# Kernel tuning notes

Hardware: AMD Instinct MI355X
Metric: run time of the kernel (lower is better)

Reference implementation:

```python
import jax, jax.numpy as jnp
import numpy as np

N_NODES = 50000
N_EDGES = 800000


def sage_conv(x, src, dst, W_l, b_l, W_r, num_nodes):
    """PyG SAGEConv with mean aggregation: out = lin_l(mean_agg(neighbors)) + lin_r(x)."""
    # gather source-node features per edge, scatter-mean into destination nodes
    msg = x[src]                                                   # [E, F]
    agg = jax.ops.segment_sum(msg, dst, num_segments=num_nodes)    # [N, F]
    cnt = jax.ops.segment_sum(jnp.ones((src.shape[0],), x.dtype), dst,
                              num_segments=num_nodes)              # [N]
    agg = agg / jnp.maximum(cnt, 1.0)[:, None]
    return agg @ W_l + b_l + x @ W_r


def setup_inputs() -> dict:
    key = jax.random.key(0)
    ks = jax.random.split(key, 8)
    d_in, d_hid, d_out = 128, 256, 128
    s = lambda k, shape, fan: jax.random.normal(k, shape, jnp.float32) / np.sqrt(fan)
    return {
        "x": jax.random.normal(ks[0], (N_NODES, d_in), jnp.float32),
        "edge_index": jax.random.randint(ks[1], (2, N_EDGES), 0, N_NODES, jnp.int64),
        "W1_l": s(ks[2], (d_in, d_hid), d_in),
        "b1": jnp.zeros((d_hid,), jnp.float32),
        "W1_r": s(ks[3], (d_in, d_hid), d_in),
        "W2_l": s(ks[4], (d_hid, d_out), d_hid),
        "b2": jnp.zeros((d_out,), jnp.float32),
        "W2_r": s(ks[5], (d_hid, d_out), d_hid),
    }


def reference(x, edge_index, W1_l, b1, W1_r, W2_l, b2, W2_r):
    src, dst = edge_index[0], edge_index[1]
    n = x.shape[0]
    h = sage_conv(x, src, dst, W1_l, b1, W1_r, n)
    h = jax.nn.relu(h)  # dropout p=0.0 -> identity
    out = sage_conv(h, src, dst, W2_l, b2, W2_r, n)
    return out
```

## Files before the change

kernel.cpp:

```cpp
#include <hip/hip_runtime.h>
#include <hip/hip_bf16.h>
#include <stdint.h>

#define NN 50000
#define NE 800000
#define NB 196
#define EPB 2048
#define NBLK ((NE + EPB - 1) / EPB)

typedef __attribute__((ext_vector_type(8))) __bf16 bf16x8;
typedef __attribute__((ext_vector_type(4))) float f32x4;
typedef __attribute__((ext_vector_type(4))) int i32x4;

__device__ __forceinline__ float bflo(uint32_t u) { return __uint_as_float(u << 16); }
__device__ __forceinline__ float bfhi(uint32_t u) { return __uint_as_float(u & 0xffff0000u); }
__device__ __forceinline__ uint16_t f2bf(float f) {
    uint32_t u = __float_as_uint(f);
    u += 0x7fffu + ((u >> 16) & 1u);
    return (uint16_t)(u >> 16);
}
__device__ __forceinline__ float bf2f(uint16_t h) { return __uint_as_float(((uint32_t)h) << 16); }

__device__ __forceinline__ int xcd_swz(int bid, int nwg) {
    int q = nwg >> 3, r = nwg & 7;
    int xcd = bid & 7, idx = bid >> 3;
    int base = (xcd < r) ? xcd * (q + 1) : r * (q + 1) + (xcd - r) * q;
    return base + idx;
}

__device__ __forceinline__ int detect_i64(const int* ei, int* sh_cnt) {
    int t = threadIdx.x;
    if (t == 0) *sh_cnt = 0;
    __syncthreads();
    if (t < 64) atomicAdd(sh_cnt, (ei[2 * t + 1] != 0) ? 1 : 0);
    __syncthreads();
    return (*sh_cnt < 4) ? 1 : 0;
}

__device__ __forceinline__ int detect_fp32(const uint32_t* xu, int* sh_cnt) {
    int t = threadIdx.x;
    if (t == 0) *sh_cnt = 0;
    __syncthreads();
    uint32_t u = xu[t & 255];
    uint32_t lo = u & 0xffffu;
    uint32_t e = (lo >> 7) & 0xffu;
    int ok = (lo == 0u) || (e >= 96u && e <= 150u);
    if (t < 256) atomicAdd(sh_cnt, ok);
    __syncthreads();
    return (*sh_cnt < 192) ? 1 : 0;
}

__global__ __launch_bounds__(256) void hist_pass(const int* __restrict__ ei,
                                                 int* __restrict__ histM) {
    __shared__ int hist[NB];
    __shared__ int shc;
    int fl = detect_i64(ei, &shc);
    for (int i = threadIdx.x; i < NB; i += 256) hist[i] = 0;
    __syncthreads();
    int base = blockIdx.x * EPB;
    for (int i = 0; i < EPB; i += 256) {
        int e = base + i + threadIdx.x;
        if (e < NE) {
            int d = fl ? ei[2 * NE + 2 * e] : ei[NE + e];
            atomicAdd(&hist[d >> 8], 1);
        }
    }
    __syncthreads();
    for (int i = threadIdx.x; i < NB; i += 256) histM[i * NBLK + blockIdx.x] = hist[i];
}

__global__ __launch_bounds__(512) void scan_rows(int* __restrict__ histM, int* __restrict__ bucket_tot) {
    __shared__ int sm[512];
    int b = blockIdx.x, t = threadIdx.x;
    int v = (t < NBLK) ? histM[b * NBLK + t] : 0;
    sm[t] = v;
    __syncthreads();
    for (int o = 1; o < 512; o <<= 1) {
        int x = (t >= o) ? sm[t - o] : 0;
        __syncthreads();
        sm[t] += x;
        __syncthreads();
    }
    if (t < NBLK) histM[b * NBLK + t] = sm[t] - v;
    if (t == 511) bucket_tot[b] = sm[511];
}

__global__ __launch_bounds__(256) void scatter_pass(const int* __restrict__ ei,
                                                    const int* __restrict__ histM,
                                                    const int* __restrict__ bucket_tot,
                                                    uint32_t* __restrict__ staging) {
    __shared__ int sm[256];
    __shared__ int curs[NB];
    __shared__ int shc;
    int fl = detect_i64(ei, &shc);
    int blk = blockIdx.x, t = threadIdx.x;
    int v = (t < NB) ? bucket_tot[t] : 0;
    sm[t] = v;
    __syncthreads();
    for (int o = 1; o < 256; o <<= 1) {
        int x = (t >= o) ? sm[t - o] : 0;
        __syncthreads();
        sm[t] += x;
        __syncthreads();
    }
    if (t < NB) curs[t] = (sm[t] - v) + histM[t * NBLK + blk];
    __syncthreads();
    int base = blk * EPB;
    for (int i = 0; i < EPB; i += 256) {
        int e = base + i + t;
        if (e < NE) {
            int s, d;
            if (fl) { s = ei[2 * e]; d = ei[2 * NE + 2 * e]; }
            else    { s = ei[e];     d = ei[NE + e]; }
            int p = atomicAdd(&curs[d >> 8], 1);
            staging[p] = ((uint32_t)(d & 0xff) << 16) | (uint32_t)s;
        }
    }
}

__global__ __launch_bounds__(256) void build_csr(const uint32_t* __restrict__ staging,
                                                 const int* __restrict__ bucket_tot,
                                                 int* __restrict__ row_start, int* __restrict__ deg,
                                                 float* __restrict__ inv_deg, int* __restrict__ csr) {
    __shared__ int degs[256];
    __shared__ int sm[256];
    __shared__ int curs[256];
    __shared__ int beg_s, cnt_s;
    int b = blockIdx.x, t = threadIdx.x;
    int v = (t < NB) ? bucket_tot[t] : 0;
    sm[t] = v;
    __syncthreads();
    for (int o = 1; o < 256; o <<= 1) {
        int x = (t >= o) ? sm[t - o] : 0;
        __syncthreads();
        sm[t] += x;
        __syncthreads();
    }
    if (t == b) { beg_s = sm[t] - v; cnt_s = v; }
    __syncthreads();
    int beg = beg_s, cnt = cnt_s;
    degs[t] = 0;
    __syncthreads();
    for (int i = t; i < cnt; i += 256) atomicAdd(&degs[(staging[beg + i] >> 16) & 0xff], 1);
    __syncthreads();
    int d = degs[t];
    sm[t] = d;
    __syncthreads();
    for (int o = 1; o < 256; o <<= 1) {
        int x = (t >= o) ? sm[t - o] : 0;
        __syncthreads();
        sm[t] += x;
        __syncthreads();
    }
    int excl = sm[t] - d;
    curs[t] = excl;
    int node = b * 256 + t;
    if (node < NN) {
        row_start[node] = beg + excl;
        deg[node] = d;
        inv_deg[node] = 1.0f / (float)(d > 0 ? d : 1);
    }
    __syncthreads();
    for (int i = t; i < cnt; i += 256) {
        uint32_t u = staging[beg + i];
        int dl = (u >> 16) & 0xff;
        int p = atomicAdd(&curs[dl], 1);
        csr[beg + p] = (int)(u & 0xffffu);
    }
}

#define NORMX_BLKS 6250
__global__ __launch_bounds__(256) void norm_all(const void* __restrict__ x,
                                                const void* __restrict__ w1l, const void* __restrict__ b1,
                                                const void* __restrict__ w1r, const void* __restrict__ w2l,
                                                const void* __restrict__ b2, const void* __restrict__ w2r,
                                                uint32_t* __restrict__ xb,
                                                uint16_t* __restrict__ w1l_sw, uint16_t* __restrict__ w1r_sw,
                                                uint16_t* __restrict__ w2l_sw, uint16_t* __restrict__ w2r_sw,
                                                uint16_t* __restrict__ bias_buf) {
    __shared__ int shc;
    int fp32 = detect_fp32((const uint32_t*)x, &shc);
    if (blockIdx.x < NORMX_BLKS) {
        int i = blockIdx.x * 256 + threadIdx.x;
        if (fp32) {
            f32x4 v = ((const f32x4*)x)[i];
            uint2 o;
            o.x = (uint32_t)f2bf(v[0]) | ((uint32_t)f2bf(v[1]) << 16);
            o.y = (uint32_t)f2bf(v[2]) | ((uint32_t)f2bf(v[3]) << 16);
            ((uint2*)xb)[i] = o;
        } else {
            ((uint2*)xb)[i] = ((const uint2*)x)[i];
        }
        return;
    }
    int tid = (blockIdx.x - NORMX_BLKS) * 256 + threadIdx.x;
    if (tid < 16384) {
        int frag = tid >> 6, lane = tid & 63;
        const void* srcw; uint16_t* dst; int N; int fl;
        if (frag < 64)       { srcw = w1l; dst = w1l_sw; N = 256; fl = frag; }
        else if (frag < 128) { srcw = w1r; dst = w1r_sw; N = 256; fl = frag - 64; }
        else if (frag < 192) { srcw = w2l; dst = w2l_sw; N = 128; fl = frag - 128; }
        else                 { srcw = w2r; dst = w2r_sw; N = 128; fl = frag - 192; }
        int NTm = N >> 4;
        int kt = fl / NTm, nt = fl - kt * NTm;
        int k0 = kt * 32 + (lane >> 4) * 8, n = nt * 16 + (lane & 15);
        uint16_t* d = dst + (size_t)fl * 512 + lane * 8;
#pragma unroll
        for (int j = 0; j < 8; j++) {
            int si = (k0 + j) * N + n;
            d[j] = fp32 ? f2bf(((const float*)srcw)[si]) : ((const uint16_t*)srcw)[si];
        }
    } else if (tid < 16384 + 384) {
        int j = tid - 16384;
        const void* s = (j < 256) ? b1 : b2;
        int jj = (j < 256) ? j : j - 256;
        bias_buf[j] = fp32 ? f2bf(((const float*)s)[jj]) : ((const uint16_t*)s)[jj];
    }
}

__global__ __launch_bounds__(256) void agg_mean_v2(const uint32_t* __restrict__ xu,
                                                   const int* __restrict__ row_start,
                                                   const int* __restrict__ deg,
                                                   const int* __restrict__ csr,
                                                   const float* __restrict__ inv_deg,
                                                   uint32_t* __restrict__ outu) {
    int wave = threadIdx.x >> 6, lane = threadIdx.x & 63;
    int half = lane >> 5, l = lane & 31;
    int node = blockIdx.x * 8 + wave * 2 + half;
    int beg = row_start[node], end = beg + deg[node];
    float lx[8], hx[8], ly[8], hy[8];
#pragma unroll
    for (int k = 0; k < 8; k++) { lx[k] = 0.f; hx[k] = 0.f; ly[k] = 0.f; hy[k] = 0.f; }
    int j = beg;
    for (; j + 8 <= end; j += 8) {
        int idx[8];
#pragma unroll
        for (int k = 0; k < 8; k++) idx[k] = csr[j + k];
#pragma unroll
        for (int k = 0; k < 8; k++) {
            uint2 v = *(const uint2*)(xu + (size_t)idx[k] * 64 + l * 2);
            lx[k] += bflo(v.x); hx[k] += bfhi(v.x);
            ly[k] += bflo(v.y); hy[k] += bfhi(v.y);
        }
    }
    for (; j < end; j++) {
        uint2 v = *(const uint2*)(xu + (size_t)csr[j] * 64 + l * 2);
        lx[0] += bflo(v.x); hx[0] += bfhi(v.x);
        ly[0] += bflo(v.y); hy[0] += bfhi(v.y);
    }
    float sc = inv_deg[node];
    float r0 = (((lx[0] + lx[1]) + (lx[2] + lx[3])) + ((lx[4] + lx[5]) + (lx[6] + lx[7]))) * sc;
    float r1 = (((hx[0] + hx[1]) + (hx[2] + hx[3])) + ((hx[4] + hx[5]) + (hx[6] + hx[7]))) * sc;
    float r2 = (((ly[0] + ly[1]) + (ly[2] + ly[3])) + ((ly[4] + ly[5]) + (ly[6] + ly[7]))) * sc;
    float r3 = (((hy[0] + hy[1]) + (hy[2] + hy[3])) + ((hy[4] + hy[5]) + (hy[6] + hy[7]))) * sc;
    uint2 o;
    o.x = (uint32_t)f2bf(r0) | ((uint32_t)f2bf(r1) << 16);
    o.y = (uint32_t)f2bf(r2) | ((uint32_t)f2bf(r3) << 16);
    *(uint2*)(outu + (size_t)node * 64 + l * 2) = o;
}

__global__ __launch_bounds__(256) void agg_final_v2(const uint32_t* __restrict__ tu,
                                                    const int* __restrict__ row_start,
                                                    const int* __restrict__ deg,
                                                    const int* __restrict__ csr,
                                                    const float* __restrict__ inv_deg,
                                                    const f32x4* __restrict__ u,
                                                    f32x4* __restrict__ out) {
    int wave = threadIdx.x >> 6, lane = threadIdx.x & 63;
    int half = lane >> 5, l = lane & 31;
    int node = blockIdx.x * 8 + wave * 2 + half;
    int beg = row_start[node], end = beg + deg[node];
    float lx[8], hx[8], ly[8], hy[8];
#pragma unroll
    for (int k = 0; k < 8; k++) { lx[k] = 0.f; hx[k] = 0.f; ly[k] = 0.f; hy[k] = 0.f; }
    int j = beg;
    for (; j + 8 <= end; j += 8) {
        int idx[8];
#pragma unroll
        for (int k = 0; k < 8; k++) idx[k] = csr[j + k];
#pragma unroll
        for (int k = 0; k < 8; k++) {
            uint2 v = *(const uint2*)(tu + (size_t)idx[k] * 64 + l * 2);
            lx[k] += bflo(v.x); hx[k] += bfhi(v.x);
            ly[k] += bflo(v.y); hy[k] += bfhi(v.y);
        }
    }
    for (; j < end; j++) {
        uint2 v = *(const uint2*)(tu + (size_t)csr[j] * 64 + l * 2);
        lx[0] += bflo(v.x); hx[0] += bfhi(v.x);
        ly[0] += bflo(v.y); hy[0] += bfhi(v.y);
    }
    float sc = inv_deg[node];
    f32x4 uv = u[(size_t)node * 32 + l];
    f32x4 r;
    r[0] = (((lx[0] + lx[1]) + (lx[2] + lx[3])) + ((lx[4] + lx[5]) + (lx[6] + lx[7]))) * sc + uv[0];
    r[1] = (((hx[0] + hx[1]) + (hx[2] + hx[3])) + ((hx[4] + hx[5]) + (hx[6] + hx[7]))) * sc + uv[1];
    r[2] = (((ly[0] + ly[1]) + (ly[2] + ly[3])) + ((ly[4] + ly[5]) + (ly[6] + ly[7]))) * sc + uv[2];
    r[3] = (((hy[0] + hy[1]) + (hy[2] + hy[3])) + ((hy[4] + hy[5]) + (hy[6] + hy[7]))) * sc + uv[3];
    out[(size_t)node * 32 + l] = r;
}

__global__ __launch_bounds__(256) void gemm1_v3(const uint16_t* __restrict__ A1,
                                                const uint16_t* __restrict__ A2,
                                                const uint16_t* __restrict__ W1sw,
                                                const uint16_t* __restrict__ W2sw,
                                                const uint16_t* __restrict__ bias,
                                                uint16_t* __restrict__ C) {
    __shared__ __align__(16) uint16_t cs[64][72];
    int wg = xcd_swz(blockIdx.x, 3128);
    int rg = wg >> 2, cg = wg & 3;
    int wave = threadIdx.x >> 6, lane = threadIdx.x & 63;
    int wr = wave >> 1, wc = wave & 1;
    int m = lane & 15, q = lane >> 4;
    int rowbase = rg * 64 + wr * 32;
    int gnt0 = cg * 4 + wc * 2;

    int ar[2];
#pragma unroll
    for (int rf = 0; rf < 2; rf++) {
        int r = rowbase + rf * 16 + m;
        ar[rf] = (r < NN) ? r : (NN - 1);
    }

    bf16x8 B1[4][2], B2[4][2];
#pragma unroll
    for (int kt = 0; kt < 4; kt++)
#pragma unroll
        for (int nt = 0; nt < 2; nt++) {
            B1[kt][nt] = *(const bf16x8*)(W1sw + ((size_t)(kt * 16 + gnt0 + nt)) * 512 + lane * 8);
            B2[kt][nt] = *(const bf16x8*)(W2sw + ((size_t)(kt * 16 + gnt0 + nt)) * 512 + lane * 8);
        }

    f32x4 acc[2][2];
#pragma unroll
    for (int rf = 0; rf < 2; rf++)
#pragma unroll
        for (int nt = 0; nt < 2; nt++)
#pragma unroll
            for (int i = 0; i < 4; i++) acc[rf][nt][i] = 0.f;

#pragma unroll
    for (int kt = 0; kt < 4; kt++) {
        bf16x8 a10 = *(const bf16x8*)(A1 + (size_t)ar[0] * 128 + kt * 32 + q * 8);
        bf16x8 a11 = *(const bf16x8*)(A1 + (size_t)ar[1] * 128 + kt * 32 + q * 8);
        bf16x8 a20 = *(const bf16x8*)(A2 + (size_t)ar[0] * 128 + kt * 32 + q * 8);
        bf16x8 a21 = *(const bf16x8*)(A2 + (size_t)ar[1] * 128 + kt * 32 + q * 8);
#pragma unroll
        for (int nt = 0; nt < 2; nt++) {
            acc[0][nt] = __builtin_amdgcn_mfma_f32_16x16x32_bf16(a10, B1[kt][nt], acc[0][nt], 0, 0, 0);
            acc[1][nt] = __builtin_amdgcn_mfma_f32_16x16x32_bf16(a11, B1[kt][nt], acc[1][nt], 0, 0, 0);
            acc[0][nt] = __builtin_amdgcn_mfma_f32_16x16x32_bf16(a20, B2[kt][nt], acc[0][nt], 0, 0, 0);
            acc[1][nt] = __builtin_amdgcn_mfma_f32_16x16x32_bf16(a21, B2[kt][nt], acc[1][nt], 0, 0, 0);
        }
    }

#pragma unroll
    for (int rf = 0; rf < 2; rf++)
#pragma unroll
        for (int nt = 0; nt < 2; nt++) {
            int coll = wc * 32 + nt * 16 + m;
            float bv = bf2f(bias[cg * 64 + coll]);
#pragma unroll
            for (int i = 0; i < 4; i++) {
                float v = fmaxf(acc[rf][nt][i] + bv, 0.f);
                cs[wr * 32 + rf * 16 + q * 4 + i][coll] = f2bf(v);
            }
        }
    __syncthreads();
    int tt = threadIdx.x;
#pragma unroll
    for (int rr = 0; rr < 2; rr++) {
        int row = rr * 32 + (tt >> 3);
        int grow = rg * 64 + row;
        if (grow < NN)
            *(i32x4*)(C + (size_t)grow * 256 + cg * 64 + (tt & 7) * 8) =
                *(const i32x4*)&cs[row][(tt & 7) * 8];
    }
}

__global__ __launch_bounds__(256) void gemm2_v3(const uint16_t* __restrict__ A,
                                                const uint16_t* __restrict__ W1sw,
                                                const uint16_t* __restrict__ W2sw,
                                                const uint16_t* __restrict__ bias,
                                                uint16_t* __restrict__ T,
                                                float* __restrict__ U) {
    __shared__ __align__(16) uint16_t ts[64][72];
    __shared__ __align__(16) float us[64][68];
    int wg = xcd_swz(blockIdx.x, 1564);
    int rg = wg >> 1, cg = wg & 1;
    int wave = threadIdx.x >> 6, lane = threadIdx.x & 63;
    int wr = wave >> 1, wc = wave & 1;
    int m = lane & 15, q = lane >> 4;
    int rowbase = rg * 64 + wr * 32;
    int gnt0 = cg * 4 + wc * 2;

    int ar[2];
#pragma unroll
    for (int rf = 0; rf < 2; rf++) {
        int r = rowbase + rf * 16 + m;
        ar[rf] = (r < NN) ? r : (NN - 1);
    }

    f32x4 acc1[2][2], acc2[2][2];
#pragma unroll
    for (int rf = 0; rf < 2; rf++)
#pragma unroll
        for (int nt = 0; nt < 2; nt++)
#pragma unroll
            for (int i = 0; i < 4; i++) { acc1[rf][nt][i] = 0.f; acc2[rf][nt][i] = 0.f; }

#pragma unroll
    for (int kt = 0; kt < 8; kt++) {
        bf16x8 b10 = *(const bf16x8*)(W1sw + ((size_t)(kt * 8 + gnt0 + 0)) * 512 + lane * 8);
        bf16x8 b11 = *(const bf16x8*)(W1sw + ((size_t)(kt * 8 + gnt0 + 1)) * 512 + lane * 8);
        bf16x8 b20 = *(const bf16x8*)(W2sw + ((size_t)(kt * 8 + gnt0 + 0)) * 512 + lane * 8);
        bf16x8 b21 = *(const bf16x8*)(W2sw + ((size_t)(kt * 8 + gnt0 + 1)) * 512 + lane * 8);
        bf16x8 a0 = *(const bf16x8*)(A + (size_t)ar[0] * 256 + kt * 32 + q * 8);
        bf16x8 a1 = *(const bf16x8*)(A + (size_t)ar[1] * 256 + kt * 32 + q * 8);
        acc1[0][0] = __builtin_amdgcn_mfma_f32_16x16x32_bf16(a0, b10, acc1[0][0], 0, 0, 0);
        acc1[0][1] = __builtin_amdgcn_mfma_f32_16x16x32_bf16(a0, b11, acc1[0][1], 0, 0, 0);
        acc1[1][0] = __builtin_amdgcn_mfma_f32_16x16x32_bf16(a1, b10, acc1[1][0], 0, 0, 0);
        acc1[1][1] = __builtin_amdgcn_mfma_f32_16x16x32_bf16(a1, b11, acc1[1][1], 0, 0, 0);
        acc2[0][0] = __builtin_amdgcn_mfma_f32_16x16x32_bf16(a0, b20, acc2[0][0], 0, 0, 0);
        acc2[0][1] = __builtin_amdgcn_mfma_f32_16x16x32_bf16(a0, b21, acc2[0][1], 0, 0, 0);
        acc2[1][0] = __builtin_amdgcn_mfma_f32_16x16x32_bf16(a1, b20, acc2[1][0], 0, 0, 0);
        acc2[1][1] = __builtin_amdgcn_mfma_f32_16x16x32_bf16(a1, b21, acc2[1][1], 0, 0, 0);
    }

#pragma unroll
    for (int rf = 0; rf < 2; rf++)
#pragma unroll
        for (int nt = 0; nt < 2; nt++) {
            int coll = wc * 32 + nt * 16 + m;
            float bv = bf2f(bias[cg * 64 + coll]);
#pragma unroll
            for (int i = 0; i < 4; i++) {
                int rl = wr * 32 + rf * 16 + q * 4 + i;
                ts[rl][coll] = f2bf(acc1[rf][nt][i]);
                us[rl][coll] = acc2[rf][nt][i] + bv;
            }
        }
    __syncthreads();
    int tt = threadIdx.x;
#pragma unroll
    for (int rr = 0; rr < 2; rr++) {
        int row = rr * 32 + (tt >> 3);
        int grow = rg * 64 + row;
        if (grow < NN)
            *(i32x4*)(T + (size_t)grow * 128 + cg * 64 + (tt & 7) * 8) =
                *(const i32x4*)&ts[row][(tt & 7) * 8];
    }
#pragma unroll
    for (int rr = 0; rr < 4; rr++) {
        int row = rr * 16 + (tt >> 4);
        int grow = rg * 64 + row;
        if (grow < NN)
            *(f32x4*)(U + (size_t)grow * 128 + cg * 64 + (tt & 15) * 4) =
                *(const f32x4*)&us[row][(tt & 15) * 4];
    }
}

extern "C" void kernel_launch(void* const* d_in, const int* in_sizes, int n_in,
                              void* d_out, int out_size, void* d_ws, size_t ws_size,
                              hipStream_t stream) {
    const void* x_raw  = d_in[0];
    const int*  ei     = (const int*)d_in[1];
    const void* W1l    = d_in[2];
    const void* b1     = d_in[3];
    const void* W1r    = d_in[4];
    const void* W2l    = d_in[5];
    const void* b2     = d_in[6];
    const void* W2r    = d_in[7];

    uint8_t* ws = (uint8_t*)d_ws;
    size_t off = 0;
    auto alloc = [&](size_t b) -> void* {
        void* p = ws + off;
        off += (b + 255) & ~(size_t)255;
        return p;
    };
    int*      histM       = (int*)alloc((size_t)NB * NBLK * 4);
    int*      bucket_tot  = (int*)alloc((NB + 4) * 4);
    int*      deg         = (int*)alloc((size_t)NN * 4);
    float*    inv_deg     = (float*)alloc((size_t)NN * 4);
    int*      row_start   = (int*)alloc((size_t)NN * 4);
    int*      csr         = (int*)alloc((size_t)NE * 4);
    uint32_t* xb          = (uint32_t*)alloc((size_t)NN * 64 * 4);
    uint16_t* bias_buf    = (uint16_t*)alloc(384 * 2);
    uint16_t* agg         = (uint16_t*)alloc((size_t)NN * 128 * 2);
    uint16_t* h           = (uint16_t*)alloc((size_t)NN * 256 * 2);
    uint16_t* t           = (uint16_t*)alloc((size_t)NN * 128 * 2);
    float*    u           = (float*)alloc((size_t)NN * 128 * 4);
    uint16_t* w1l_sw      = (uint16_t*)alloc(128 * 256 * 2);
    uint16_t* w1r_sw      = (uint16_t*)alloc(128 * 256 * 2);
    uint16_t* w2l_sw      = (uint16_t*)alloc(256 * 128 * 2);
    uint16_t* w2r_sw      = (uint16_t*)alloc(256 * 128 * 2);

    uint32_t* staging = (uint32_t*)h;

    hist_pass<<<NBLK, 256, 0, stream>>>(ei, histM);
    scan_rows<<<NB, 512, 0, stream>>>(histM, bucket_tot);
    scatter_pass<<<NBLK, 256, 0, stream>>>(ei, histM, bucket_tot, staging);
    build_csr<<<NB, 256, 0, stream>>>(staging, bucket_tot, row_start, deg, inv_deg, csr);

    norm_all<<<NORMX_BLKS + 66, 256, 0, stream>>>(x_raw, W1l, b1, W1r, W2l, b2, W2r,
                                                  xb, w1l_sw, w1r_sw, w2l_sw, w2r_sw, bias_buf);

    agg_mean_v2<<<NN / 8, 256, 0, stream>>>(xb, row_start, deg, csr, inv_deg, (uint32_t*)agg);
    gemm1_v3<<<3128, 256, 0, stream>>>(agg, (const uint16_t*)xb, w1l_sw, w1r_sw, bias_buf, h);
    gemm2_v3<<<1564, 256, 0, stream>>>(h, w2l_sw, w2r_sw, bias_buf + 256, t, u);
    agg_final_v2<<<NN / 8, 256, 0, stream>>>((const uint32_t*)t, row_start, deg, csr, inv_deg,
                                             (const f32x4*)u, (f32x4*)d_out);
}
```

Baseline: 268.3 us.

## Fuse layer-1 mean aggregation into the first GEMM via shared-memory tile

Replaces the separate agg_mean and gemm1 kernels with one kernel. Each 64-node block first gathers and averages neighbour features into a shared-memory tile, then runs the MFMA GEMM against both weight matrices, covering all 256 output columns per block. This removes the global round-trip of the aggregated matrix and one launch. In exchange the grid shrinks to about 782 blocks, weights are reloaded per k-step instead of held in registers, and the gather phase interleaves two nodes per half-wave, which raises register pressure and could lower occupancy.

```diff
diff --git a/kernel.cpp b/kernel.cpp
--- a/kernel.cpp
+++ b/kernel.cpp
@@ -218,163 +218,167 @@
     }
 }
 
-__global__ __launch_bounds__(256) void agg_mean_v2(const uint32_t* __restrict__ xu,
-                                                   const int* __restrict__ row_start,
-                                                   const int* __restrict__ deg,
-                                                   const int* __restrict__ csr,
-                                                   const float* __restrict__ inv_deg,
-                                                   uint32_t* __restrict__ outu) {
-    int wave = threadIdx.x >> 6, lane = threadIdx.x & 63;
-    int half = lane >> 5, l = lane & 31;
-    int node = blockIdx.x * 8 + wave * 2 + half;
-    int beg = row_start[node], end = beg + deg[node];
-    float lx[8], hx[8], ly[8], hy[8];
-#pragma unroll
-    for (int k = 0; k < 8; k++) { lx[k] = 0.f; hx[k] = 0.f; ly[k] = 0.f; hy[k] = 0.f; }
-    int j = beg;
-    for (; j + 8 <= end; j += 8) {
-        int idx[8];
-#pragma unroll
-        for (int k = 0; k < 8; k++) idx[k] = csr[j + k];
-#pragma unroll
-        for (int k = 0; k < 8; k++) {
-            uint2 v = *(const uint2*)(xu + (size_t)idx[k] * 64 + l * 2);
-            lx[k] += bflo(v.x); hx[k] += bfhi(v.x);
-            ly[k] += bflo(v.y); hy[k] += bfhi(v.y);
-        }
-    }
-    for (; j < end; j++) {
-        uint2 v = *(const uint2*)(xu + (size_t)csr[j] * 64 + l * 2);
-        lx[0] += bflo(v.x); hx[0] += bfhi(v.x);
-        ly[0] += bflo(v.y); hy[0] += bfhi(v.y);
-    }
-    float sc = inv_deg[node];
-    float r0 = (((lx[0] + lx[1]) + (lx[2] + lx[3])) + ((lx[4] + lx[5]) + (lx[6] + lx[7]))) * sc;
-    float r1 = (((hx[0] + hx[1]) + (hx[2] + hx[3])) + ((hx[4] + hx[5]) + (hx[6] + hx[7]))) * sc;
-    float r2 = (((ly[0] + ly[1]) + (ly[2] + ly[3])) + ((ly[4] + ly[5]) + (ly[6] + ly[7]))) * sc;
-    float r3 = (((hy[0] + hy[1]) + (hy[2] + hy[3])) + ((hy[4] + hy[5]) + (hy[6] + hy[7]))) * sc;
-    uint2 o;
-    o.x = (uint32_t)f2bf(r0) | ((uint32_t)f2bf(r1) << 16);
-    o.y = (uint32_t)f2bf(r2) | ((uint32_t)f2bf(r3) << 16);
-    *(uint2*)(outu + (size_t)node * 64 + l * 2) = o;
-}
-
-__global__ __launch_bounds__(256) void agg_final_v2(const uint32_t* __restrict__ tu,
-                                                    const int* __restrict__ row_start,
-                                                    const int* __restrict__ deg,
-                                                    const int* __restrict__ csr,
-                                                    const float* __restrict__ inv_deg,
-                                                    const f32x4* __restrict__ u,
-                                                    f32x4* __restrict__ out) {
-    int wave = threadIdx.x >> 6, lane = threadIdx.x & 63;
-    int half = lane >> 5, l = lane & 31;
-    int node = blockIdx.x * 8 + wave * 2 + half;
-    int beg = row_start[node], end = beg + deg[node];
-    float lx[8], hx[8], ly[8], hy[8];
-#pragma unroll
-    for (int k = 0; k < 8; k++) { lx[k] = 0.f; hx[k] = 0.f; ly[k] = 0.f; hy[k] = 0.f; }
-    int j = beg;
-    for (; j + 8 <= end; j += 8) {
-        int idx[8];
-#pragma unroll
-        for (int k = 0; k < 8; k++) idx[k] = csr[j + k];
-#pragma unroll
-        for (int k = 0; k < 8; k++) {
-            uint2 v = *(const uint2*)(tu + (size_t)idx[k] * 64 + l * 2);
-            lx[k] += bflo(v.x); hx[k] += bfhi(v.x);
-            ly[k] += bflo(v.y); hy[k] += bfhi(v.y);
-        }
-    }
-    for (; j < end; j++) {
-        uint2 v = *(const uint2*)(tu + (size_t)csr[j] * 64 + l * 2);
-        lx[0] += bflo(v.x); hx[0] += bfhi(v.x);
-        ly[0] += bflo(v.y); hy[0] += bfhi(v.y);
-    }
-    float sc = inv_deg[node];
-    f32x4 uv = u[(size_t)node * 32 + l];
-    f32x4 r;
-    r[0] = (((lx[0] + lx[1]) + (lx[2] + lx[3])) + ((lx[4] + lx[5]) + (lx[6] + lx[7]))) * sc + uv[0];
-    r[1] = (((hx[0] + hx[1]) + (hx[2] + hx[3])) + ((hx[4] + hx[5]) + (hx[6] + hx[7]))) * sc + uv[1];
-    r[2] = (((ly[0] + ly[1]) + (ly[2] + ly[3])) + ((ly[4] + ly[5]) + (ly[6] + ly[7]))) * sc + uv[2];
-    r[3] = (((hy[0] + hy[1]) + (hy[2] + hy[3])) + ((hy[4] + hy[5]) + (hy[6] + hy[7]))) * sc + uv[3];
-    out[(size_t)node * 32 + l] = r;
-}
-
-__global__ __launch_bounds__(256) void gemm1_v3(const uint16_t* __restrict__ A1,
-                                                const uint16_t* __restrict__ A2,
+#define ATW 136
+__global__ __launch_bounds__(256) void fused_l1(const uint32_t* __restrict__ xu,
+                                                const int* __restrict__ row_start,
+                                                const int* __restrict__ deg,
+                                                const int* __restrict__ csr,
+                                                const float* __restrict__ inv_deg,
+                                                const uint16_t* __restrict__ xb16,
                                                 const uint16_t* __restrict__ W1sw,
                                                 const uint16_t* __restrict__ W2sw,
                                                 const uint16_t* __restrict__ bias,
-                                                uint16_t* __restrict__ C) {
-    __shared__ __align__(16) uint16_t cs[64][72];
-    int wg = xcd_swz(blockIdx.x, 3128);
-    int rg = wg >> 2, cg = wg & 3;
-    int wave = threadIdx.x >> 6, lane = threadIdx.x & 63;
+                                                uint16_t* __restrict__ H) {
+    __shared__ __align__(16) uint16_t atile[64][ATW];
+    __shared__ __align__(16) uint16_t stg[64][136];
+    int node0 = blockIdx.x * 64;
+    int tid = threadIdx.x;
+    int wave = tid >> 6, lane = tid & 63;
+    int half = lane >> 5, l = lane & 31;
+
+    for (int pp = 0; pp < 4; pp++) {
+        int nlA = wave * 16 + pp * 4 + half * 2;
+        int nlB = nlA + 1;
+        int na = node0 + nlA; na = (na < NN) ? na : (NN - 1);
+        int nb = node0 + nlB; nb = (nb < NN) ? nb : (NN - 1);
+        int begA = row_start[na], endA = begA + deg[na];
+        int begB = row_start[nb], endB = begB + deg[nb];
+        float alx[8], ahx[8], aly[8], ahy[8];
+        float blx[8], bhx[8], bly[8], bhy[8];
+#pragma unroll
+        for (int k = 0; k < 8; k++) {
+            alx[k] = 0.f; ahx[k] = 0.f; aly[k] = 0.f; ahy[k] = 0.f;
+            blx[k] = 0.f; bhx[k] = 0.f; bly[k] = 0.f; bhy[k] = 0.f;
+        }
+        int ja = begA, jb = begB;
+        for (; ja + 8 <= endA && jb + 8 <= endB; ja += 8, jb += 8) {
+            int ia[8], ib[8];
+#pragma unroll
+            for (int k = 0; k < 8; k++) { ia[k] = csr[ja + k]; ib[k] = csr[jb + k]; }
+#pragma unroll
+            for (int k = 0; k < 8; k++) {
+                uint2 va = *(const uint2*)(xu + (size_t)ia[k] * 64 + l * 2);
+                uint2 vb = *(const uint2*)(xu + (size_t)ib[k] * 64 + l * 2);
+                alx[k] += bflo(va.x); ahx[k] += bfhi(va.x);
+                aly[k] += bflo(va.y); ahy[k] += bfhi(va.y);
+                blx[k] += bflo(vb.x); bhx[k] += bfhi(vb.x);
+                bly[k] += bflo(vb.y); bhy[k] += bfhi(vb.y);
+            }
+        }
+        for (; ja + 8 <= endA; ja += 8) {
+            int ia[8];
+#pragma unroll
+            for (int k = 0; k < 8; k++) ia[k] = csr[ja + k];
+#pragma unroll
+            for (int k = 0; k < 8; k++) {
+                uint2 va = *(const uint2*)(xu + (size_t)ia[k] * 64 + l * 2);
+                alx[k] += bflo(va.x); ahx[k] += bfhi(va.x);
+                aly[k] += bflo(va.y); ahy[k] += bfhi(va.y);
+            }
+        }
+        for (; jb + 8 <= endB; jb += 8) {
+            int ib[8];
+#pragma unroll
+            for (int k = 0; k < 8; k++) ib[k] = csr[jb + k];
+#pragma unroll
+            for (int k = 0; k < 8; k++) {
+                uint2 vb = *(const uint2*)(xu + (size_t)ib[k] * 64 + l * 2);
+                blx[k] += bflo(vb.x); bhx[k] += bfhi(vb.x);
+                bly[k] += bflo(vb.y); bhy[k] += bfhi(vb.y);
+            }
+        }
+        for (; ja < endA; ja++) {
+            uint2 va = *(const uint2*)(xu + (size_t)csr[ja] * 64 + l * 2);
+            alx[0] += bflo(va.x); ahx[0] += bfhi(va.x);
+            aly[0] += bflo(va.y); ahy[0] += bfhi(va.y);
+        }
+        for (; jb < endB; jb++) {
+            uint2 vb = *(const uint2*)(xu + (size_t)csr[jb] * 64 + l * 2);
+            blx[0] += bflo(vb.x); bhx[0] += bfhi(vb.x);
+            bly[0] += bflo(vb.y); bhy[0] += bfhi(vb.y);
+        }
+        float sa = inv_deg[na], sb = inv_deg[nb];
+        float a0 = (((alx[0] + alx[1]) + (alx[2] + alx[3])) + ((alx[4] + alx[5]) + (alx[6] + alx[7]))) * sa;
+        float a1 = (((ahx[0] + ahx[1]) + (ahx[2] + ahx[3])) + ((ahx[4] + ahx[5]) + (ahx[6] + ahx[7]))) * sa;
+        float a2 = (((aly[0] + aly[1]) + (aly[2] + aly[3])) + ((aly[4] + aly[5]) + (aly[6] + aly[7]))) * sa;
+        float a3 = (((ahy[0] + ahy[1]) + (ahy[2] + ahy[3])) + ((ahy[4] + ahy[5]) + (ahy[6] + ahy[7]))) * sa;
+        float b0 = (((blx[0] + blx[1]) + (blx[2] + blx[3])) + ((blx[4] + blx[5]) + (blx[6] + blx[7]))) * sb;
+        float b1v = (((bhx[0] + bhx[1]) + (bhx[2] + bhx[3])) + ((bhx[4] + bhx[5]) + (bhx[6] + bhx[7]))) * sb;
+        float b2v = (((bly[0] + bly[1]) + (bly[2] + bly[3])) + ((bly[4] + bly[5]) + (bly[6] + bly[7]))) * sb;
+        float b3 = (((bhy[0] + bhy[1]) + (bhy[2] + bhy[3])) + ((bhy[4] + bhy[5]) + (bhy[6] + bhy[7]))) * sb;
+        uint2 oa, ob;
+        oa.x = (uint32_t)f2bf(a0) | ((uint32_t)f2bf(a1) << 16);
+        oa.y = (uint32_t)f2bf(a2) | ((uint32_t)f2bf(a3) << 16);
+        ob.x = (uint32_t)f2bf(b0) | ((uint32_t)f2bf(b1v) << 16);
+        ob.y = (uint32_t)f2bf(b2v) | ((uint32_t)f2bf(b3) << 16);
+        *(uint2*)((char*)&atile[nlA][0] + l * 8) = oa;
+        *(uint2*)((char*)&atile[nlB][0] + l * 8) = ob;
+    }
+    __syncthreads();
+
     int wr = wave >> 1, wc = wave & 1;
     int m = lane & 15, q = lane >> 4;
-    int rowbase = rg * 64 + wr * 32;
-    int gnt0 = cg * 4 + wc * 2;
-
     int ar[2];
 #pragma unroll
     for (int rf = 0; rf < 2; rf++) {
-        int r = rowbase + rf * 16 + m;
+        int r = node0 + wr * 32 + rf * 16 + m;
         ar[rf] = (r < NN) ? r : (NN - 1);
     }
-
-    bf16x8 B1[4][2], B2[4][2];
-#pragma unroll
-    for (int kt = 0; kt < 4; kt++)
-#pragma unroll
-        for (int nt = 0; nt < 2; nt++) {
-            B1[kt][nt] = *(const bf16x8*)(W1sw + ((size_t)(kt * 16 + gnt0 + nt)) * 512 + lane * 8);
-            B2[kt][nt] = *(const bf16x8*)(W2sw + ((size_t)(kt * 16 + gnt0 + nt)) * 512 + lane * 8);
-        }
-
-    f32x4 acc[2][2];
+    f32x4 acc[2][8];
 #pragma unroll
     for (int rf = 0; rf < 2; rf++)
 #pragma unroll
-        for (int nt = 0; nt < 2; nt++)
+        for (int nt = 0; nt < 8; nt++)
 #pragma unroll
             for (int i = 0; i < 4; i++) acc[rf][nt][i] = 0.f;
 
 #pragma unroll
     for (int kt = 0; kt < 4; kt++) {
-        bf16x8 a10 = *(const bf16x8*)(A1 + (size_t)ar[0] * 128 + kt * 32 + q * 8);
-        bf16x8 a11 = *(const bf16x8*)(A1 + (size_t)ar[1] * 128 + kt * 32 + q * 8);
-        bf16x8 a20 = *(const bf16x8*)(A2 + (size_t)ar[0] * 128 + kt * 32 + q * 8);
-        bf16x8 a21 = *(const bf16x8*)(A2 + (size_t)ar[1] * 128 + kt * 32 + q * 8);
-#pragma unroll
-        for (int nt = 0; nt < 2; nt++) {
-            acc[0][nt] = __builtin_amdgcn_mfma_f32_16x16x32_bf16(a10, B1[kt][nt], acc[0][nt], 0, 0, 0);
-            acc[1][nt] = __builtin_amdgcn_mfma_f32_16x16x32_bf16(a11, B1[kt][nt], acc[1][nt], 0, 0, 0);
-            acc[0][nt] = __builtin_amdgcn_mfma_f32_16x16x32_bf16(a20, B2[kt][nt], acc[0][nt], 0, 0, 0);
-            acc[1][nt] = __builtin_amdgcn_mfma_f32_16x16x32_bf16(a21, B2[kt][nt], acc[1][nt], 0, 0, 0);
-        }
-    }
-
-#pragma unroll
-    for (int rf = 0; rf < 2; rf++)
-#pragma unroll
-        for (int nt = 0; nt < 2; nt++) {
-            int coll = wc * 32 + nt * 16 + m;
-            float bv = bf2f(bias[cg * 64 + coll]);
-#pragma unroll
-            for (int i = 0; i < 4; i++) {
-                float v = fmaxf(acc[rf][nt][i] + bv, 0.f);
-                cs[wr * 32 + rf * 16 + q * 4 + i][coll] = f2bf(v);
+        bf16x8 a1f[2], a2f[2];
+#pragma unroll
+        for (int rf = 0; rf < 2; rf++) {
+            a1f[rf] = *(const bf16x8*)((const char*)atile +
+                        (size_t)(wr * 32 + rf * 16 + m) * (ATW * 2) + kt * 64 + q * 16);
+            a2f[rf] = *(const bf16x8*)(xb16 + (size_t)ar[rf] * 128 + kt * 32 + q * 8);
+        }
+#pragma unroll
+        for (int nt = 0; nt < 8; nt++) {
+            int gnt = wc * 8 + nt;
+            bf16x8 B1 = *(const bf16x8*)(W1sw + ((size_t)(kt * 16 + gnt)) * 512 + lane * 8);
+            bf16x8 B2 = *(const bf16x8*)(W2sw + ((size_t)(kt * 16 + gnt)) * 512 + lane * 8);
+            acc[0][nt] = __builtin_amdgcn_mfma_f32_16x16x32_bf16(a1f[0], B1, acc[0][nt], 0, 0, 0);
+            acc[1][nt] = __builtin_amdgcn_mfma_f32_16x16x32_bf16(a1f[1], B1, acc[1][nt], 0, 0, 0);
+            acc[0][nt] = __builtin_amdgcn_mfma_f32_16x16x32_bf16(a2f[0], B2, acc[0][nt], 0, 0, 0);
+            acc[1][nt] = __builtin_amdgcn_mfma_f32_16x16x32_bf16(a2f[1], B2, acc[1][nt], 0, 0, 0);
+        }
+    }
+
+#pragma unroll
+    for (int r = 0; r < 2; r++) {
+        if (wc == r) {
+#pragma unroll
+            for (int nt = 0; nt < 8; nt++) {
+                int cl = nt * 16 + m;
+                float bv = bf2f(bias[r * 128 + cl]);
+#pragma unroll
+                for (int rf = 0; rf < 2; rf++)
+#pragma unroll
+                    for (int i = 0; i < 4; i++) {
+                        float v = fmaxf(acc[rf][nt][i] + bv, 0.f);
+                        stg[wr * 32 + rf * 16 + q * 4 + i][cl] = f2bf(v);
+                    }
             }
         }
-    __syncthreads();
-    int tt = threadIdx.x;
-#pragma unroll
-    for (int rr = 0; rr < 2; rr++) {
-        int row = rr * 32 + (tt >> 3);
-        int grow = rg * 64 + row;
-        if (grow < NN)
-            *(i32x4*)(C + (size_t)grow * 256 + cg * 64 + (tt & 7) * 8) =
-                *(const i32x4*)&cs[row][(tt & 7) * 8];
+        __syncthreads();
+#pragma unroll
+        for (int rr = 0; rr < 4; rr++) {
+            int row = rr * 16 + (tid >> 4);
+            int grow = node0 + row;
+            if (grow < NN)
+                *(i32x4*)(H + (size_t)grow * 256 + r * 128 + (tid & 15) * 8) =
+                    *(const i32x4*)&stg[row][(tid & 15) * 8];
+        }
+        __syncthreads();
     }
 }
 
@@ -460,6 +464,47 @@
     }
 }
 
+__global__ __launch_bounds__(256) void agg_final_v2(const uint32_t* __restrict__ tu,
+                                                    const int* __restrict__ row_start,
+                                                    const int* __restrict__ deg,
+                                                    const int* __restrict__ csr,
+                                                    const float* __restrict__ inv_deg,
+                                                    const f32x4* __restrict__ u,
+                                                    f32x4* __restrict__ out) {
+    int wave = threadIdx.x >> 6, lane = threadIdx.x & 63;
+    int half = lane >> 5, l = lane & 31;
+    int node = blockIdx.x * 8 + wave * 2 + half;
+    int beg = row_start[node], end = beg + deg[node];
+    float lx[8], hx[8], ly[8], hy[8];
+#pragma unroll
+    for (int k = 0; k < 8; k++) { lx[k] = 0.f; hx[k] = 0.f; ly[k] = 0.f; hy[k] = 0.f; }
+    int j = beg;
+    for (; j + 8 <= end; j += 8) {
+        int idx[8];
+#pragma unroll
+        for (int k = 0; k < 8; k++) idx[k] = csr[j + k];
+#pragma unroll
+        for (int k = 0; k < 8; k++) {
+            uint2 v = *(const uint2*)(tu + (size_t)idx[k] * 64 + l * 2);
+            lx[k] += bflo(v.x); hx[k] += bfhi(v.x);
+            ly[k] += bflo(v.y); hy[k] += bfhi(v.y);
+        }
+    }
+    for (; j < end; j++) {
+        uint2 v = *(const uint2*)(tu + (size_t)csr[j] * 64 + l * 2);
+        lx[0] += bflo(v.x); hx[0] += bfhi(v.x);
+        ly[0] += bflo(v.y); hy[0] += bfhi(v.y);
+    }
+    float sc = inv_deg[node];
+    f32x4 uv = u[(size_t)node * 32 + l];
+    f32x4 r;
+    r[0] = (((lx[0] + lx[1]) + (lx[2] + lx[3])) + ((lx[4] + lx[5]) + (lx[6] + lx[7]))) * sc + uv[0];
+    r[1] = (((hx[0] + hx[1]) + (hx[2] + hx[3])) + ((hx[4] + hx[5]) + (hx[6] + hx[7]))) * sc + uv[1];
+    r[2] = (((ly[0] + ly[1]) + (ly[2] + ly[3])) + ((ly[4] + ly[5]) + (ly[6] + ly[7]))) * sc + uv[2];
+    r[3] = (((hy[0] + hy[1]) + (hy[2] + hy[3])) + ((hy[4] + hy[5]) + (hy[6] + hy[7]))) * sc + uv[3];
+    out[(size_t)node * 32 + l] = r;
+}
+
 extern "C" void kernel_launch(void* const* d_in, const int* in_sizes, int n_in,
                               void* d_out, int out_size, void* d_ws, size_t ws_size,
                               hipStream_t stream) {
@@ -487,7 +532,6 @@
     int*      csr         = (int*)alloc((size_t)NE * 4);
     uint32_t* xb          = (uint32_t*)alloc((size_t)NN * 64 * 4);
     uint16_t* bias_buf    = (uint16_t*)alloc(384 * 2);
-    uint16_t* agg         = (uint16_t*)alloc((size_t)NN * 128 * 2);
     uint16_t* h           = (uint16_t*)alloc((size_t)NN * 256 * 2);
     uint16_t* t           = (uint16_t*)alloc((size_t)NN * 128 * 2);
     float*    u           = (float*)alloc((size_t)NN * 128 * 4);
@@ -506,8 +550,8 @@
     norm_all<<<NORMX_BLKS + 66, 256, 0, stream>>>(x_raw, W1l, b1, W1r, W2l, b2, W2r,
                                                   xb, w1l_sw, w1r_sw, w2l_sw, w2r_sw, bias_buf);
 
-    agg_mean_v2<<<NN / 8, 256, 0, stream>>>(xb, row_start, deg, csr, inv_deg, (uint32_t*)agg);
-    gemm1_v3<<<3128, 256, 0, stream>>>(agg, (const uint16_t*)xb, w1l_sw, w1r_sw, bias_buf, h);
+    fused_l1<<<(NN + 63) / 64, 256, 0, stream>>>(xb, row_start, deg, csr, inv_deg,
+                                                 (const uint16_t*)xb, w1l_sw, w1r_sw, bias_buf, h);
     gemm2_v3<<<1564, 256, 0, stream>>>(h, w2l_sw, w2r_sw, bias_buf + 256, t, u);
     agg_final_v2<<<NN / 8, 256, 0, stream>>>((const uint32_t*)t, row_start, deg, csr, inv_deg,
                                              (const f32x4*)u, (f32x4*)d_out);
```

New measurement: 303.0 us. +13.0%, slower.

## Replace CSR build scan pipeline with fixed-capacity buckets and merge into norm kernel

Applied to the files above, without the earlier changes.

The CSR construction used hist, scan, scatter and build kernels. It is now a single scatter kernel in which each block reserves space through global atomics on per-bucket cursors, with every bucket given a fixed-capacity 8192-slot region. CSR building is fused into the conversion/normalization kernel as extra blocks, which removes two launches and the global prefix scans. The risk is overflow if any bucket exceeds 8192 edges. That holds for uniform random graphs but is not guaranteed in general, and edge order within a node now depends on atomic timing.

```diff
diff --git a/kernel.cpp b/kernel.cpp
--- a/kernel.cpp
+++ b/kernel.cpp
@@ -7,6 +7,7 @@
 #define NB 196
 #define EPB 2048
 #define NBLK ((NE + EPB - 1) / EPB)
+#define BCAP 8192
 
 typedef __attribute__((ext_vector_type(8))) __bf16 bf16x8;
 typedef __attribute__((ext_vector_type(4))) float f32x4;
@@ -50,138 +51,96 @@
     return (*sh_cnt < 192) ? 1 : 0;
 }
 
-__global__ __launch_bounds__(256) void hist_pass(const int* __restrict__ ei,
-                                                 int* __restrict__ histM) {
+__global__ __launch_bounds__(256) void scatter1(const int* __restrict__ ei,
+                                                int* __restrict__ bucket_cur,
+                                                uint32_t* __restrict__ staging) {
     __shared__ int hist[NB];
+    __shared__ int curs[NB];
     __shared__ int shc;
     int fl = detect_i64(ei, &shc);
-    for (int i = threadIdx.x; i < NB; i += 256) hist[i] = 0;
+    int t = threadIdx.x;
+    for (int i = t; i < NB; i += 256) hist[i] = 0;
     __syncthreads();
     int base = blockIdx.x * EPB;
     for (int i = 0; i < EPB; i += 256) {
-        int e = base + i + threadIdx.x;
+        int e = base + i + t;
         if (e < NE) {
             int d = fl ? ei[2 * NE + 2 * e] : ei[NE + e];
             atomicAdd(&hist[d >> 8], 1);
         }
     }
     __syncthreads();
-    for (int i = threadIdx.x; i < NB; i += 256) histM[i * NBLK + blockIdx.x] = hist[i];
-}
-
-__global__ __launch_bounds__(512) void scan_rows(int* __restrict__ histM, int* __restrict__ bucket_tot) {
-    __shared__ int sm[512];
-    int b = blockIdx.x, t = threadIdx.x;
-    int v = (t < NBLK) ? histM[b * NBLK + t] : 0;
-    sm[t] = v;
-    __syncthreads();
-    for (int o = 1; o < 512; o <<= 1) {
-        int x = (t >= o) ? sm[t - o] : 0;
-        __syncthreads();
-        sm[t] += x;
-        __syncthreads();
-    }
-    if (t < NBLK) histM[b * NBLK + t] = sm[t] - v;
-    if (t == 511) bucket_tot[b] = sm[511];
-}
-
-__global__ __launch_bounds__(256) void scatter_pass(const int* __restrict__ ei,
-                                                    const int* __restrict__ histM,
-                                                    const int* __restrict__ bucket_tot,
-                                                    uint32_t* __restrict__ staging) {
-    __shared__ int sm[256];
-    __shared__ int curs[NB];
-    __shared__ int shc;
-    int fl = detect_i64(ei, &shc);
-    int blk = blockIdx.x, t = threadIdx.x;
-    int v = (t < NB) ? bucket_tot[t] : 0;
-    sm[t] = v;
-    __syncthreads();
-    for (int o = 1; o < 256; o <<= 1) {
-        int x = (t >= o) ? sm[t - o] : 0;
-        __syncthreads();
-        sm[t] += x;
-        __syncthreads();
-    }
-    if (t < NB) curs[t] = (sm[t] - v) + histM[t * NBLK + blk];
-    __syncthreads();
-    int base = blk * EPB;
+    for (int i = t; i < NB; i += 256)
+        curs[i] = (hist[i] > 0) ? atomicAdd(&bucket_cur[i], hist[i]) : 0;
+    __syncthreads();
     for (int i = 0; i < EPB; i += 256) {
         int e = base + i + t;
         if (e < NE) {
             int s, d;
             if (fl) { s = ei[2 * e]; d = ei[2 * NE + 2 * e]; }
             else    { s = ei[e];     d = ei[NE + e]; }
-            int p = atomicAdd(&curs[d >> 8], 1);
-            staging[p] = ((uint32_t)(d & 0xff) << 16) | (uint32_t)s;
-        }
-    }
-}
-
-__global__ __launch_bounds__(256) void build_csr(const uint32_t* __restrict__ staging,
-                                                 const int* __restrict__ bucket_tot,
-                                                 int* __restrict__ row_start, int* __restrict__ deg,
-                                                 float* __restrict__ inv_deg, int* __restrict__ csr) {
-    __shared__ int degs[256];
-    __shared__ int sm[256];
-    __shared__ int curs[256];
-    __shared__ int beg_s, cnt_s;
-    int b = blockIdx.x, t = threadIdx.x;
-    int v = (t < NB) ? bucket_tot[t] : 0;
-    sm[t] = v;
-    __syncthreads();
-    for (int o = 1; o < 256; o <<= 1) {
-        int x = (t >= o) ? sm[t - o] : 0;
-        __syncthreads();
-        sm[t] += x;
-        __syncthreads();
-    }
-    if (t == b) { beg_s = sm[t] - v; cnt_s = v; }
-    __syncthreads();
-    int beg = beg_s, cnt = cnt_s;
-    degs[t] = 0;
-    __syncthreads();
-    for (int i = t; i < cnt; i += 256) atomicAdd(&degs[(staging[beg + i] >> 16) & 0xff], 1);
-    __syncthreads();
-    int d = degs[t];
-    sm[t] = d;
-    __syncthreads();
-    for (int o = 1; o < 256; o <<= 1) {
-        int x = (t >= o) ? sm[t - o] : 0;
-        __syncthreads();
-        sm[t] += x;
-        __syncthreads();
-    }
-    int excl = sm[t] - d;
-    curs[t] = excl;
-    int node = b * 256 + t;
-    if (node < NN) {
-        row_start[node] = beg + excl;
-        deg[node] = d;
-        inv_deg[node] = 1.0f / (float)(d > 0 ? d : 1);
-    }
-    __syncthreads();
-    for (int i = t; i < cnt; i += 256) {
-        uint32_t u = staging[beg + i];
-        int dl = (u >> 16) & 0xff;
-        int p = atomicAdd(&curs[dl], 1);
-        csr[beg + p] = (int)(u & 0xffffu);
+            int b = d >> 8;
+            int p = atomicAdd(&curs[b], 1);
+            staging[b * BCAP + p] = ((uint32_t)(d & 0xff) << 16) | (uint32_t)s;
+        }
     }
 }
 
 #define NORMX_BLKS 6250
-__global__ __launch_bounds__(256) void norm_all(const void* __restrict__ x,
+__global__ __launch_bounds__(256) void csr_norm(const uint32_t* __restrict__ staging,
+                                                const int* __restrict__ bucket_cur,
+                                                const void* __restrict__ x,
                                                 const void* __restrict__ w1l, const void* __restrict__ b1,
                                                 const void* __restrict__ w1r, const void* __restrict__ w2l,
                                                 const void* __restrict__ b2, const void* __restrict__ w2r,
+                                                int* __restrict__ row_start, int* __restrict__ deg,
+                                                float* __restrict__ inv_deg, int* __restrict__ csr,
                                                 uint32_t* __restrict__ xb,
                                                 uint16_t* __restrict__ w1l_sw, uint16_t* __restrict__ w1r_sw,
                                                 uint16_t* __restrict__ w2l_sw, uint16_t* __restrict__ w2r_sw,
                                                 uint16_t* __restrict__ bias_buf) {
+    int blk = blockIdx.x;
+    int t = threadIdx.x;
+    if (blk < NB) {
+        __shared__ int degs[256];
+        __shared__ int sm[256];
+        __shared__ int curs[256];
+        int beg = blk * BCAP, cnt = bucket_cur[blk];
+        degs[t] = 0;
+        __syncthreads();
+        for (int i = t; i < cnt; i += 256) atomicAdd(&degs[(staging[beg + i] >> 16) & 0xff], 1);
+        __syncthreads();
+        int d = degs[t];
+        sm[t] = d;
+        __syncthreads();
+        for (int o = 1; o < 256; o <<= 1) {
+            int x2 = (t >= o) ? sm[t - o] : 0;
+            __syncthreads();
+            sm[t] += x2;
+            __syncthreads();
+        }
+        int excl = sm[t] - d;
+        curs[t] = excl;
+        int node = blk * 256 + t;
+        if (node < NN) {
+            row_start[node] = beg + excl;
+            deg[node] = d;
+            inv_deg[node] = 1.0f / (float)(d > 0 ? d : 1);
+        }
+        __syncthreads();
+        for (int i = t; i < cnt; i += 256) {
+            uint32_t u = staging[beg + i];
+            int dl = (u >> 16) & 0xff;
+            int p = atomicAdd(&curs[dl], 1);
+            csr[beg + p] = (int)(u & 0xffffu);
+        }
+        return;
+    }
     __shared__ int shc;
     int fp32 = detect_fp32((const uint32_t*)x, &shc);
-    if (blockIdx.x < NORMX_BLKS) {
-        int i = blockIdx.x * 256 + threadIdx.x;
+    int nb = blk - NB;
+    if (nb < NORMX_BLKS) {
+        int i = nb * 256 + t;
         if (fp32) {
             f32x4 v = ((const f32x4*)x)[i];
             uint2 o;
@@ -193,7 +152,7 @@
         }
         return;
     }
-    int tid = (blockIdx.x - NORMX_BLKS) * 256 + threadIdx.x;
+    int tid = (nb - NORMX_BLKS) * 256 + t;
     if (tid < 16384) {
         int frag = tid >> 6, lane = tid & 63;
         const void* srcw; uint16_t* dst; int N; int fl;
@@ -479,12 +438,11 @@
         off += (b + 255) & ~(size_t)255;
         return p;
     };
-    int*      histM       = (int*)alloc((size_t)NB * NBLK * 4);
-    int*      bucket_tot  = (int*)alloc((NB + 4) * 4);
+    int*      bucket_cur  = (int*)alloc((NB + 4) * 4);
     int*      deg         = (int*)alloc((size_t)NN * 4);
     float*    inv_deg     = (float*)alloc((size_t)NN * 4);
     int*      row_start   = (int*)alloc((size_t)NN * 4);
-    int*      csr         = (int*)alloc((size_t)NE * 4);
+    int*      csr         = (int*)alloc((size_t)NB * BCAP * 4);
     uint32_t* xb          = (uint32_t*)alloc((size_t)NN * 64 * 4);
     uint16_t* bias_buf    = (uint16_t*)alloc(384 * 2);
     uint16_t* agg         = (uint16_t*)alloc((size_t)NN * 128 * 2);
@@ -498,13 +456,12 @@
 
     uint32_t* staging = (uint32_t*)h;
 
-    hist_pass<<<NBLK, 256, 0, stream>>>(ei, histM);
-    scan_rows<<<NB, 512, 0, stream>>>(histM, bucket_tot);
-    scatter_pass<<<NBLK, 256, 0, stream>>>(ei, histM, bucket_tot, staging);
-    build_csr<<<NB, 256, 0, stream>>>(staging, bucket_tot, row_start, deg, inv_deg, csr);
-
-    norm_all<<<NORMX_BLKS + 66, 256, 0, stream>>>(x_raw, W1l, b1, W1r, W2l, b2, W2r,
-                                                  xb, w1l_sw, w1r_sw, w2l_sw, w2r_sw, bias_buf);
+    hipMemsetAsync(bucket_cur, 0, NB * 4, stream);
+    scatter1<<<NBLK, 256, 0, stream>>>(ei, bucket_cur, staging);
+    csr_norm<<<NB + NORMX_BLKS + 66, 256, 0, stream>>>(staging, bucket_cur, x_raw,
+                                                       W1l, b1, W1r, W2l, b2, W2r,
+                                                       row_start, deg, inv_deg, csr,
+                                                       xb, w1l_sw, w1r_sw, w2l_sw, w2r_sw, bias_buf);
 
     agg_mean_v2<<<NN / 8, 256, 0, stream>>>(xb, row_start, deg, csr, inv_deg, (uint32_t*)agg);
     gemm1_v3<<<3128, 256, 0, stream>>>(agg, (const uint16_t*)xb, w1l_sw, w1r_sw, bias_buf, h);
```

After: 255.6 us. 1.05x faster.
